# Performance work log

Hardware: AMD Instinct MI355X
Metric: run time of the kernel (lower is better)

The kernel has to match this reference:

```python
import jax, jax.numpy as jnp
import numpy as np

FEATURE_DIM = 768
LAMBDA_REG = 0.01
NUM_ITERS = 5
LR = 0.1
SIGMA = 2.0
MARGIN = 1.0
BN_EPS = 1e-5


def setup_inputs() -> dict:
    key = jax.random.key(0)
    ks = jax.random.split(key, 10)
    B, D = 32, FEATURE_DIM
    search_features = jax.random.normal(ks[0], (B, D, 32, 32), dtype=jnp.float32)
    target_features = jax.random.normal(ks[1], (B, D, 16, 16), dtype=jnp.float32)
    target_mask = jax.random.uniform(ks[2], (B, 1, 16, 16), dtype=jnp.float32)
    conv_w = jax.random.normal(ks[3], (D, D), dtype=jnp.float32) * (1.0 / np.sqrt(D))
    conv_b = jax.random.normal(ks[4], (D,), dtype=jnp.float32) * 0.01
    bn_gamma = jnp.ones((D,), dtype=jnp.float32)
    bn_beta = jnp.zeros((D,), dtype=jnp.float32)
    bn_mean = jax.random.normal(ks[5], (D,), dtype=jnp.float32) * 0.01
    bn_var = jax.random.uniform(ks[6], (D,), dtype=jnp.float32, minval=0.5, maxval=1.5)
    filter_init = jax.random.normal(ks[7], (1, D, 1, 1), dtype=jnp.float32) * 0.01
    return {
        "search_features": search_features,
        "target_features": target_features,
        "target_mask": target_mask,
        "conv_w": conv_w,
        "conv_b": conv_b,
        "bn_gamma": bn_gamma,
        "bn_beta": bn_beta,
        "bn_mean": bn_mean,
        "bn_var": bn_var,
        "filter_init": filter_init,
    }


def _proj(x, conv_w, conv_b, bn_gamma, bn_beta, bn_mean, bn_var):
    # 1x1 conv == channel-wise GEMM, then BatchNorm (eval mode, running stats)
    y = jnp.einsum('bdhw,ed->behw', x, conv_w) + conv_b[None, :, None, None]
    inv_std = bn_gamma / jnp.sqrt(bn_var + BN_EPS)
    return (y - bn_mean[None, :, None, None]) * inv_std[None, :, None, None] + bn_beta[None, :, None, None]


def _gaussian_label(mask):
    B, _, H, W = mask.shape
    yy, xx = jnp.meshgrid(jnp.arange(H, dtype=jnp.float32), jnp.arange(W, dtype=jnp.float32), indexing='ij')
    yy = yy[None, None]  # (1,1,H,W)
    xx = xx[None, None]
    msum = jnp.clip(mask.sum(axis=(2, 3), keepdims=True), 1.0)
    cy = (mask * yy).sum(axis=(2, 3), keepdims=True) / msum
    cx = (mask * xx).sum(axis=(2, 3), keepdims=True) / msum
    return jnp.exp(-((xx - cx) ** 2 + (yy - cy) ** 2) / (2.0 * SIGMA ** 2))


def reference(search_features, target_features, target_mask, conv_w, conv_b,
              bn_gamma, bn_beta, bn_mean, bn_var, filter_init):
    sp = _proj(search_features, conv_w, conv_b, bn_gamma, bn_beta, bn_mean, bn_var)
    tp = _proj(target_features, conv_w, conv_b, bn_gamma, bn_beta, bn_mean, bn_var)
    B = tp.shape[0]
    label = _gaussian_label(target_mask)  # (B,1,H',W')
    f = jnp.broadcast_to(filter_init, (B,) + filter_init.shape[1:])  # (B,D,1,1)
    for _ in range(NUM_ITERS):
        response = (tp * f).sum(axis=1, keepdims=True)  # (B,1,H',W')
        loss = jnp.maximum(MARGIN - response * label, 0.0)
        grad = jnp.where(loss > 0, -label * target_mask, 0.0)
        grad = grad.mean(axis=(2, 3), keepdims=True)  # (B,1,1,1), broadcasts over D
        f = f - LR * (grad + LAMBDA_REG * f)
    return (sp * f).sum(axis=1, keepdims=True)  # (B,1,H,W)
```

## Files before the change

### kernel.cpp

```cpp
#include <hip/hip_runtime.h>
#include <math.h>

#define DD   768
#define BB   32
#define NTP  256
#define NSP  1024
#define NT   (BB*NTP)
#define NS   (BB*NSP)
#define ECH  16
#define CHE  (DD/ECH)

#define OFF_UP  0
#define OFF_VP  (OFF_UP + ECH*DD)
#define OFF_K   (OFF_VP + ECH*DD)
#define OFF_TR0 (OFF_K + 64)
#define OFF_TS0 (OFF_TR0 + NT)
#define OFF_SR  (OFF_TS0 + NT)
#define OFF_SS  (OFF_SR + NS)

#define A5 0.99500999000499900f

__global__ void k_prep(const float* __restrict__ w, const float* __restrict__ cb,
                       const float* __restrict__ gamma, const float* __restrict__ beta,
                       const float* __restrict__ mean, const float* __restrict__ var,
                       const float* __restrict__ fi, float* __restrict__ ws) {
    int bx = blockIdx.x;
    int t = threadIdx.x;
    if (bx < ECH) {
        __shared__ float wu[CHE], wv[CHE];
        if (t < CHE) {
            int e = bx * CHE + t;
            float inv = gamma[e] / sqrtf(var[e] + 1e-5f);
            wv[t] = inv;
            wu[t] = inv * fi[e];
        }
        __syncthreads();
        if (t < 192) {
            const float4* w4 = (const float4*)w;
            float4 Ru = {0,0,0,0}, Rv = {0,0,0,0};
            #pragma unroll
            for (int j = 0; j < CHE; ++j) {
                float4 x = w4[(size_t)(bx * CHE + j) * 192 + t];
                float a = wu[j], b = wv[j];
                Ru.x += x.x * a; Ru.y += x.y * a; Ru.z += x.z * a; Ru.w += x.w * a;
                Rv.x += x.x * b; Rv.y += x.y * b; Rv.z += x.z * b; Rv.w += x.w * b;
            }
            *(float4*)(ws + OFF_UP + bx * DD + t * 4) = Ru;
            *(float4*)(ws + OFF_VP + bx * DD + t * 4) = Rv;
        }
    } else {
        __shared__ float r1[256], r2[256];
        float a1 = 0.f, a2 = 0.f;
        for (int e = t; e < DD; e += 256) {
            float inv = gamma[e] / sqrtf(var[e] + 1e-5f);
            float x = (cb[e] - mean[e]) * inv + beta[e];
            a1 += x * fi[e];
            a2 += x;
        }
        r1[t] = a1; r2[t] = a2;
        __syncthreads();
        for (int s = 128; s > 0; s >>= 1) {
            if (t < s) { r1[t] += r1[t + s]; r2[t] += r2[t + s]; }
            __syncthreads();
        }
        if (t == 0) { ws[OFF_K] = r1[0]; ws[OFF_K + 1] = r2[0]; }
    }
}

__global__ __launch_bounds__(256) void k_big(const float* __restrict__ sf,
                                             const float* __restrict__ tf,
                                             float* __restrict__ ws) {
    int bx = blockIdx.x;
    int t = threadIdx.x;
    int pxf4 = t & 31, sub = t >> 5;
    __shared__ float su[DD], sv[DD];
    if (t < 192) {
        float4 U = {0,0,0,0}, V = {0,0,0,0};
        #pragma unroll
        for (int ec = 0; ec < ECH; ++ec) {
            float4 a = ((const float4*)(ws + OFF_UP + ec * DD))[t];
            float4 b = ((const float4*)(ws + OFF_VP + ec * DD))[t];
            U.x += a.x; U.y += a.y; U.z += a.z; U.w += a.w;
            V.x += b.x; V.y += b.y; V.z += b.z; V.w += b.w;
        }
        ((float4*)su)[t] = U;
        ((float4*)sv)[t] = V;
    }
    __syncthreads();

    const float4* base;
    int STR;
    float4 *oR, *oS;
    if (bx < 256) {
        int b = bx >> 3, q = bx & 7;
        base = (const float4*)sf + ((size_t)b * DD + sub * 96) * (NSP/4) + q * 32 + pxf4;
        STR = NSP / 4;
        int g4 = b * 256 + q * 32 + pxf4;
        oR = (float4*)(ws + OFF_SR) + g4;
        oS = (float4*)(ws + OFF_SS) + g4;
    } else {
        int u = bx - 256;
        int b = u >> 1, q = u & 1;
        base = (const float4*)tf + ((size_t)b * DD + sub * 96) * (NTP/4) + q * 32 + pxf4;
        STR = NTP / 4;
        int g4 = b * 64 + q * 32 + pxf4;
        oR = (float4*)(ws + OFF_TR0) + g4;
        oS = (float4*)(ws + OFF_TS0) + g4;
    }

    float4 accR = {0,0,0,0}, accS = {0,0,0,0};
    float4 buf[12];
    #pragma unroll
    for (int k = 0; k < 12; ++k) buf[k] = base[(size_t)k * STR];
    #pragma unroll
    for (int g = 1; g < 8; ++g) {
        float4 nxt[12];
        #pragma unroll
        for (int k = 0; k < 12; ++k) nxt[k] = base[(size_t)(g * 12 + k) * STR];
        #pragma unroll
        for (int k = 0; k < 12; ++k) {
            int ch = sub * 96 + (g - 1) * 12 + k;
            float u = su[ch], v = sv[ch];
            accR.x += buf[k].x * u; accR.y += buf[k].y * u; accR.z += buf[k].z * u; accR.w += buf[k].w * u;
            accS.x += buf[k].x * v; accS.y += buf[k].y * v; accS.z += buf[k].z * v; accS.w += buf[k].w * v;
            buf[k] = nxt[k];
        }
    }
    #pragma unroll
    for (int k = 0; k < 12; ++k) {
        int ch = sub * 96 + 84 + k;
        float u = su[ch], v = sv[ch];
        accR.x += buf[k].x * u; accR.y += buf[k].y * u; accR.z += buf[k].z * u; accR.w += buf[k].w * u;
        accS.x += buf[k].x * v; accS.y += buf[k].y * v; accS.z += buf[k].z * v; accS.w += buf[k].w * v;
    }

    __shared__ float4 redR[8][32], redS[8][32];
    redR[sub][pxf4] = accR; redS[sub][pxf4] = accS;
    __syncthreads();
    for (int s = 4; s > 0; s >>= 1) {
        if (sub < s) {
            float4 a = redR[sub + s][pxf4], m = redR[sub][pxf4];
            m.x += a.x; m.y += a.y; m.z += a.z; m.w += a.w; redR[sub][pxf4] = m;
            float4 c = redS[sub + s][pxf4], n = redS[sub][pxf4];
            n.x += c.x; n.y += c.y; n.z += c.z; n.w += c.w; redS[sub][pxf4] = n;
        }
        __syncthreads();
    }
    if (sub == 0) { *oR = redR[0][pxf4]; *oS = redS[0][pxf4]; }
}

__global__ void k_final(const float* __restrict__ mask, const float* __restrict__ ws,
                        float* __restrict__ out) {
    int b = blockIdx.x;
    int p = threadIdx.x;
    int lane = p & 63, wv = p >> 6;
    int h = p >> 4, w = p & 15;
    float K1 = ws[OFF_K], K2 = ws[OFF_K + 1];
    float r0 = K1 + ws[OFF_TR0 + b * 256 + p];
    float s0 = K2 + ws[OFF_TS0 + b * 256 + p];
    float m = mask[b * 256 + p];
    __shared__ float cross[4];
    auto bsum = [&](float v) -> float {
        #pragma unroll
        for (int o = 32; o > 0; o >>= 1) v += __shfl_xor(v, o, 64);
        if (lane == 0) cross[wv] = v;
        __syncthreads();
        float r = cross[0] + cross[1] + cross[2] + cross[3];
        __syncthreads();
        return r;
    };
    float msum = bsum(m);
    float sy = bsum(m * (float)h);
    float sx = bsum(m * (float)w);
    msum = fmaxf(msum, 1.0f);
    float cy = sy / msum, cx = sx / msum;
    float dx = (float)w - cx, dy = (float)h - cy;
    float label = expf(-(dx * dx + dy * dy) * 0.125f);
    float A = 1.0f, c = 0.0f;
    const float decay = 1.0f - 0.1f * 0.01f;
    #pragma unroll
    for (int it = 0; it < 5; ++it) {
        float resp = A * r0 + c * s0;
        float gc = (1.0f - resp * label > 0.0f) ? (-label * m) : 0.0f;
        float g = bsum(gc) * (1.0f / 256.0f);
        c = decay * c - 0.1f * g;
        A *= decay;
    }
    int g4 = b * 256 + p;
    float4 R = ((const float4*)(ws + OFF_SR))[g4];
    float4 S = ((const float4*)(ws + OFF_SS))[g4];
    float4 o;
    o.x = A5 * (K1 + R.x) + c * (K2 + S.x);
    o.y = A5 * (K1 + R.y) + c * (K2 + S.y);
    o.z = A5 * (K1 + R.z) + c * (K2 + S.z);
    o.w = A5 * (K1 + R.w) + c * (K2 + S.w);
    ((float4*)out)[g4] = o;
}

extern "C" void kernel_launch(void* const* d_in, const int* in_sizes, int n_in,
                              void* d_out, int out_size, void* d_ws, size_t ws_size,
                              hipStream_t stream) {
    const float* sf    = (const float*)d_in[0];
    const float* tf    = (const float*)d_in[1];
    const float* mask  = (const float*)d_in[2];
    const float* w     = (const float*)d_in[3];
    const float* cb    = (const float*)d_in[4];
    const float* gamma = (const float*)d_in[5];
    const float* beta  = (const float*)d_in[6];
    const float* mean  = (const float*)d_in[7];
    const float* var   = (const float*)d_in[8];
    const float* fi    = (const float*)d_in[9];
    float* out = (float*)d_out;
    float* ws  = (float*)d_ws;

    k_prep <<<ECH + 1, 256, 0, stream>>>(w, cb, gamma, beta, mean, var, fi, ws);
    k_big  <<<320,     256, 0, stream>>>(sf, tf, ws);
    k_final<<<BB,      256, 0, stream>>>(mask, ws, out);
}
```

Baseline: 35.92 us.

## Split channel reduction across four grid blocks per tile for more parallelism

The big streaming kernel now splits the 768-channel reduction into four quarters, each handled by its own block, so the launch grows from 320 to 1280 blocks, with launch bounds asking for more occupancy. Partial results for each quarter are written to separate workspace slices and summed in the final kernel. This raises the number of in-flight memory requests on a bandwidth-bound streaming pass that previously underfilled the GPU's compute units. In exchange there are four times as many partial outputs to write and read back, and a shorter per-thread prefetch pipeline.

```diff
diff --git a/kernel.cpp b/kernel.cpp
--- a/kernel.cpp
+++ b/kernel.cpp
@@ -9,14 +9,16 @@
 #define NS   (BB*NSP)
 #define ECH  16
 #define CHE  (DD/ECH)
+#define NQ   4
+#define QCH  (DD/NQ)
 
 #define OFF_UP  0
 #define OFF_VP  (OFF_UP + ECH*DD)
 #define OFF_K   (OFF_VP + ECH*DD)
 #define OFF_TR0 (OFF_K + 64)
-#define OFF_TS0 (OFF_TR0 + NT)
-#define OFF_SR  (OFF_TS0 + NT)
-#define OFF_SS  (OFF_SR + NS)
+#define OFF_TS0 (OFF_TR0 + NQ*NT)
+#define OFF_SR  (OFF_TS0 + NQ*NT)
+#define OFF_SS  (OFF_SR + NQ*NS)
 
 #define A5 0.99500999000499900f
 
@@ -67,21 +69,26 @@
     }
 }
 
-__global__ __launch_bounds__(256) void k_big(const float* __restrict__ sf,
-                                             const float* __restrict__ tf,
-                                             float* __restrict__ ws) {
+__global__ __launch_bounds__(256, 5) void k_big(const float* __restrict__ sf,
+                                                const float* __restrict__ tf,
+                                                float* __restrict__ ws) {
     int bx = blockIdx.x;
     int t = threadIdx.x;
     int pxf4 = t & 31, sub = t >> 5;
-    __shared__ float su[DD], sv[DD];
-    if (t < 192) {
+
+    int b, q, cq; bool isS;
+    if (bx < 1024) { isS = true;  cq = bx & 3; q = (bx >> 2) & 7; b = bx >> 5; }
+    else           { isS = false; int u = bx - 1024; cq = u & 3; q = (u >> 2) & 1; b = u >> 3; }
+
+    __shared__ float su[QCH], sv[QCH];
+    if (t < QCH / 4) {
         float4 U = {0,0,0,0}, V = {0,0,0,0};
         #pragma unroll
         for (int ec = 0; ec < ECH; ++ec) {
-            float4 a = ((const float4*)(ws + OFF_UP + ec * DD))[t];
-            float4 b = ((const float4*)(ws + OFF_VP + ec * DD))[t];
+            float4 a = ((const float4*)(ws + OFF_UP))[ec * 192 + cq * 48 + t];
+            float4 c = ((const float4*)(ws + OFF_VP))[ec * 192 + cq * 48 + t];
             U.x += a.x; U.y += a.y; U.z += a.z; U.w += a.w;
-            V.x += b.x; V.y += b.y; V.z += b.z; V.w += b.w;
+            V.x += c.x; V.y += c.y; V.z += c.z; V.w += c.w;
         }
         ((float4*)su)[t] = U;
         ((float4*)sv)[t] = V;
@@ -91,35 +98,32 @@
     const float4* base;
     int STR;
     float4 *oR, *oS;
-    if (bx < 256) {
-        int b = bx >> 3, q = bx & 7;
-        base = (const float4*)sf + ((size_t)b * DD + sub * 96) * (NSP/4) + q * 32 + pxf4;
+    if (isS) {
+        base = (const float4*)sf + ((size_t)b * DD + cq * QCH + sub * 24) * (NSP/4) + q * 32 + pxf4;
         STR = NSP / 4;
         int g4 = b * 256 + q * 32 + pxf4;
-        oR = (float4*)(ws + OFF_SR) + g4;
-        oS = (float4*)(ws + OFF_SS) + g4;
+        oR = (float4*)(ws + OFF_SR) + cq * (NS/4) + g4;
+        oS = (float4*)(ws + OFF_SS) + cq * (NS/4) + g4;
     } else {
-        int u = bx - 256;
-        int b = u >> 1, q = u & 1;
-        base = (const float4*)tf + ((size_t)b * DD + sub * 96) * (NTP/4) + q * 32 + pxf4;
+        base = (const float4*)tf + ((size_t)b * DD + cq * QCH + sub * 24) * (NTP/4) + q * 32 + pxf4;
         STR = NTP / 4;
         int g4 = b * 64 + q * 32 + pxf4;
-        oR = (float4*)(ws + OFF_TR0) + g4;
-        oS = (float4*)(ws + OFF_TS0) + g4;
+        oR = (float4*)(ws + OFF_TR0) + cq * (NT/4) + g4;
+        oS = (float4*)(ws + OFF_TS0) + cq * (NT/4) + g4;
     }
 
     float4 accR = {0,0,0,0}, accS = {0,0,0,0};
-    float4 buf[12];
-    #pragma unroll
-    for (int k = 0; k < 12; ++k) buf[k] = base[(size_t)k * STR];
-    #pragma unroll
-    for (int g = 1; g < 8; ++g) {
-        float4 nxt[12];
-        #pragma unroll
-        for (int k = 0; k < 12; ++k) nxt[k] = base[(size_t)(g * 12 + k) * STR];
-        #pragma unroll
-        for (int k = 0; k < 12; ++k) {
-            int ch = sub * 96 + (g - 1) * 12 + k;
+    float4 buf[8];
+    #pragma unroll
+    for (int k = 0; k < 8; ++k) buf[k] = base[(size_t)k * STR];
+    #pragma unroll
+    for (int g = 1; g < 3; ++g) {
+        float4 nxt[8];
+        #pragma unroll
+        for (int k = 0; k < 8; ++k) nxt[k] = base[(size_t)(g * 8 + k) * STR];
+        #pragma unroll
+        for (int k = 0; k < 8; ++k) {
+            int ch = sub * 24 + (g - 1) * 8 + k;
             float u = su[ch], v = sv[ch];
             accR.x += buf[k].x * u; accR.y += buf[k].y * u; accR.z += buf[k].z * u; accR.w += buf[k].w * u;
             accS.x += buf[k].x * v; accS.y += buf[k].y * v; accS.z += buf[k].z * v; accS.w += buf[k].w * v;
@@ -127,8 +131,8 @@
         }
     }
     #pragma unroll
-    for (int k = 0; k < 12; ++k) {
-        int ch = sub * 96 + 84 + k;
+    for (int k = 0; k < 8; ++k) {
+        int ch = sub * 24 + 16 + k;
         float u = su[ch], v = sv[ch];
         accR.x += buf[k].x * u; accR.y += buf[k].y * u; accR.z += buf[k].z * u; accR.w += buf[k].w * u;
         accS.x += buf[k].x * v; accS.y += buf[k].y * v; accS.z += buf[k].z * v; accS.w += buf[k].w * v;
@@ -156,8 +160,12 @@
     int lane = p & 63, wv = p >> 6;
     int h = p >> 4, w = p & 15;
     float K1 = ws[OFF_K], K2 = ws[OFF_K + 1];
-    float r0 = K1 + ws[OFF_TR0 + b * 256 + p];
-    float s0 = K2 + ws[OFF_TS0 + b * 256 + p];
+    float r0 = K1, s0 = K2;
+    #pragma unroll
+    for (int cq = 0; cq < NQ; ++cq) {
+        r0 += ws[OFF_TR0 + cq * NT + b * 256 + p];
+        s0 += ws[OFF_TS0 + cq * NT + b * 256 + p];
+    }
     float m = mask[b * 256 + p];
     __shared__ float cross[4];
     auto bsum = [&](float v) -> float {
@@ -187,13 +195,19 @@
         A *= decay;
     }
     int g4 = b * 256 + p;
-    float4 R = ((const float4*)(ws + OFF_SR))[g4];
-    float4 S = ((const float4*)(ws + OFF_SS))[g4];
+    float4 R = {K1, K1, K1, K1}, S = {K2, K2, K2, K2};
+    #pragma unroll
+    for (int cq = 0; cq < NQ; ++cq) {
+        float4 a = ((const float4*)(ws + OFF_SR))[cq * (NS/4) + g4];
+        float4 d = ((const float4*)(ws + OFF_SS))[cq * (NS/4) + g4];
+        R.x += a.x; R.y += a.y; R.z += a.z; R.w += a.w;
+        S.x += d.x; S.y += d.y; S.z += d.z; S.w += d.w;
+    }
     float4 o;
-    o.x = A5 * (K1 + R.x) + c * (K2 + S.x);
-    o.y = A5 * (K1 + R.y) + c * (K2 + S.y);
-    o.z = A5 * (K1 + R.z) + c * (K2 + S.z);
-    o.w = A5 * (K1 + R.w) + c * (K2 + S.w);
+    o.x = A5 * R.x + c * S.x;
+    o.y = A5 * R.y + c * S.y;
+    o.z = A5 * R.z + c * S.z;
+    o.w = A5 * R.w + c * S.w;
     ((float4*)out)[g4] = o;
 }
 
@@ -214,6 +228,6 @@
     float* ws  = (float*)d_ws;
 
     k_prep <<<ECH + 1, 256, 0, stream>>>(w, cb, gamma, beta, mean, var, fi, ws);
-    k_big  <<<320,     256, 0, stream>>>(sf, tf, ws);
+    k_big  <<<1280,    256, 0, stream>>>(sf, tf, ws);
     k_final<<<BB,      256, 0, stream>>>(mask, ws, out);
 }
```

New measurement: 34.61 us. 3.6% less time.
